# Kernel tuning notes

Measured on AMD Instinct MI355X. Metric: run time of the kernel, lower is better.

## Reference

```python
import jax, jax.numpy as jnp
import numpy as np

B, N, C, H, L, WSZ = 4, 16384, 1024, 16, 256, 512
Dh = C // H
Nb = N // B
NW = Nb // WSZ
EPS = 1e-6
SCALE = Dh ** -0.5


def _ln(h, g=None, b=None):
    m = h.mean(-1, keepdims=True)
    v = h.var(-1, keepdims=True)
    h = (h - m) * jax.lax.rsqrt(v + EPS)
    if g is not None:
        h = h * g + b
    return h


def setup_inputs() -> dict:
    key = jax.random.key(0)
    ks = jax.random.split(key, 16)
    s = 0.02
    return {
        'x': jax.random.normal(ks[0], (N, C), jnp.float32),
        'context': jax.random.normal(ks[1], (B, L, C), jnp.float32),
        'mod': jax.random.normal(ks[2], (B, C), jnp.float32),
        'W_mod': jax.random.normal(ks[3], (C, 6 * C), jnp.float32) * s,
        'b_mod': jnp.zeros((6 * C,), jnp.float32),
        'gamma2': jnp.ones((C,), jnp.float32),
        'beta2': jnp.zeros((C,), jnp.float32),
        'W_qkv': jax.random.normal(ks[4], (C, 3 * C), jnp.float32) * s,
        'b_qkv': jnp.zeros((3 * C,), jnp.float32),
        'W_so': jax.random.normal(ks[5], (C, C), jnp.float32) * s,
        'b_so': jnp.zeros((C,), jnp.float32),
        'W_q': jax.random.normal(ks[6], (C, C), jnp.float32) * s,
        'b_q': jnp.zeros((C,), jnp.float32),
        'W_kv': jax.random.normal(ks[7], (C, 2 * C), jnp.float32) * s,
        'b_kv': jnp.zeros((2 * C,), jnp.float32),
        'W_co': jax.random.normal(ks[8], (C, C), jnp.float32) * s,
        'b_co': jnp.zeros((C,), jnp.float32),
        'W_m1': jax.random.normal(ks[9], (C, 4 * C), jnp.float32) * s,
        'b_m1': jnp.zeros((4 * C,), jnp.float32),
        'W_m2': jax.random.normal(ks[10], (4 * C, C), jnp.float32) * s,
        'b_m2': jnp.zeros((C,), jnp.float32),
    }


def reference(x, context, mod, W_mod, b_mod, gamma2, beta2, W_qkv, b_qkv,
              W_so, b_so, W_q, b_q, W_kv, b_kv, W_co, b_co,
              W_m1, b_m1, W_m2, b_m2):
    xb = x.reshape(B, Nb, C)

    # AdaLN modulation: SiLU -> Linear -> 6 chunks, broadcast per batch item
    m6 = jax.nn.silu(mod) @ W_mod + b_mod                   # [B, 6C]
    sh_msa, sc_msa, g_msa, sh_mlp, sc_mlp, g_mlp = jnp.split(m6, 6, axis=-1)

    # --- windowed sparse self-attention ---
    h = _ln(xb) * (1.0 + sc_msa[:, None]) + sh_msa[:, None]
    qkv = (h @ W_qkv + b_qkv).reshape(B, NW, WSZ, 3, H, Dh)
    q, k, v = qkv[:, :, :, 0], qkv[:, :, :, 1], qkv[:, :, :, 2]
    a = jax.nn.softmax(jnp.einsum('bwqhd,bwkhd->bwhqk', q, k) * SCALE, axis=-1)
    o = jnp.einsum('bwhqk,bwkhd->bwqhd', a, v).reshape(B, Nb, C)
    xb = xb + g_msa[:, None] * (o @ W_so + b_so)

    # --- full cross-attention to per-batch context ---
    h = _ln(xb, gamma2, beta2)
    q = (h @ W_q + b_q).reshape(B, Nb, H, Dh)
    kv = (context @ W_kv + b_kv).reshape(B, L, 2, H, Dh)
    k, v = kv[:, :, 0], kv[:, :, 1]
    a = jax.nn.softmax(jnp.einsum('bqhd,bkhd->bhqk', q, k) * SCALE, axis=-1)
    o = jnp.einsum('bhqk,bkhd->bqhd', a, v).reshape(B, Nb, C)
    xb = xb + (o @ W_co + b_co)

    # --- modulated sparse FFN ---
    h = _ln(xb) * (1.0 + sc_mlp[:, None]) + sh_mlp[:, None]
    h = jax.nn.gelu(h @ W_m1 + b_m1, approximate=True)
    xb = xb + g_mlp[:, None] * (h @ W_m2 + b_m2)

    return xb.reshape(N, C)
```

## Files before the change

### kernel.cpp

```cpp
#include <hip/hip_runtime.h>

typedef unsigned short u16;
typedef __attribute__((ext_vector_type(8))) short short8;
typedef __attribute__((ext_vector_type(4))) float f32x4;

#define SCALE_ 0.125f

struct __align__(8) U16x4 { u16 x, y, z, w; };

__device__ __forceinline__ u16 f2b(float f) {
  union { float f; unsigned u; } c; c.f = f;
  unsigned u = c.u;
  u += 0x7fffu + ((u >> 16) & 1u);
  return (u16)(u >> 16);
}

__device__ __forceinline__ void gload16(const void* g, void* l) {
  __builtin_amdgcn_global_load_lds((const __attribute__((address_space(1))) void*)g,
                                   (__attribute__((address_space(3))) void*)l,
                                   16, 0, 0);
}

__device__ __forceinline__ float gelu_t(float x) {
  float z = 1.5957691216057308f * (x + 0.044715f * x * x * x);
  return x / (1.0f + __expf(-z));
}

__global__ __launch_bounds__(256) void wcast(const float* __restrict__ W,
                                             u16* __restrict__ Wt, int K, int N) {
  __shared__ float t[32][33];
  const int nb = N >> 5;
  const int k0 = (blockIdx.x / nb) << 5;
  const int n0 = (blockIdx.x % nb) << 5;
  const int tx = threadIdx.x & 31;
  const int ty = threadIdx.x >> 5;
#pragma unroll
  for (int r = 0; r < 32; r += 8) t[ty + r][tx] = W[(size_t)(k0 + ty + r) * N + n0 + tx];
  __syncthreads();
#pragma unroll
  for (int r = 0; r < 32; r += 8) Wt[(size_t)(n0 + ty + r) * K + k0 + tx] = f2b(t[tx][ty + r]);
}

__global__ __launch_bounds__(256) void cast_bf(const float* __restrict__ in,
                                               u16* __restrict__ out) {
  const int i = blockIdx.x * 256 + threadIdx.x;
  const float4 v = ((const float4*)in)[i];
  U16x4 o; o.x = f2b(v.x); o.y = f2b(v.y); o.z = f2b(v.z); o.w = f2b(v.w);
  ((U16x4*)out)[i] = o;
}

__global__ __launch_bounds__(256) void mod_gemm(const float* __restrict__ mod,
                                                const float* __restrict__ Wm,
                                                const float* __restrict__ bm,
                                                float* __restrict__ m6) {
  __shared__ float s[4096];
  for (int i = threadIdx.x; i < 4096; i += 256) {
    float x = mod[i];
    s[i] = x / (1.0f + __expf(-x));
  }
  __syncthreads();
  const int j = blockIdx.x * 256 + threadIdx.x;
  float a0 = bm[j], a1 = a0, a2 = a0, a3 = a0;
#pragma unroll 8
  for (int c = 0; c < 1024; c++) {
    float w = Wm[(size_t)c * 6144 + j];
    a0 += s[c] * w;
    a1 += s[1024 + c] * w;
    a2 += s[2048 + c] * w;
    a3 += s[3072 + c] * w;
  }
  m6[j] = a0; m6[6144 + j] = a1; m6[12288 + j] = a2; m6[18432 + j] = a3;
}

__global__ __launch_bounds__(256) void ln_k(const float* __restrict__ x,
                                            u16* __restrict__ out,
                                            const float* __restrict__ g,
                                            const float* __restrict__ bb,
                                            int batch_stride, int add_one) {
  const int row = blockIdx.x;
  const int tid = threadIdx.x;
  const float4 v = ((const float4*)(x + (size_t)row * 1024))[tid];
  float s = v.x + v.y + v.z + v.w;
  float q = v.x * v.x + v.y * v.y + v.z * v.z + v.w * v.w;
#pragma unroll
  for (int m = 1; m < 64; m <<= 1) {
    s += __shfl_xor(s, m, 64);
    q += __shfl_xor(q, m, 64);
  }
  __shared__ float ps[4], pq[4];
  if ((tid & 63) == 0) { ps[tid >> 6] = s; pq[tid >> 6] = q; }
  __syncthreads();
  s = ps[0] + ps[1] + ps[2] + ps[3];
  q = pq[0] + pq[1] + pq[2] + pq[3];
  const float mean = s * (1.0f / 1024.0f);
  const float var = q * (1.0f / 1024.0f) - mean * mean;
  const float rstd = rsqrtf(var + 1e-6f);
  const int batch = row >> 12;
  const float4 gv = ((const float4*)(g + (size_t)batch * batch_stride))[tid];
  const float4 bv = ((const float4*)(bb + (size_t)batch * batch_stride))[tid];
  const float ao = add_one ? 1.0f : 0.0f;
  U16x4 o;
  o.x = f2b((v.x - mean) * rstd * (gv.x + ao) + bv.x);
  o.y = f2b((v.y - mean) * rstd * (gv.y + ao) + bv.y);
  o.z = f2b((v.z - mean) * rstd * (gv.z + ao) + bv.z);
  o.w = f2b((v.w - mean) * rstd * (gv.w + ao) + bv.w);
  ((U16x4*)(out + (size_t)row * 1024))[tid] = o;
}

template <int EPI>
__global__ __launch_bounds__(256) void gemm_bt(const u16* __restrict__ A,
                                               const u16* __restrict__ Bt,
                                               const float* __restrict__ bias,
                                               void* outp, const float* res,
                                               const float* gate, int M, int N,
                                               int K, int gate_stride) {
  __shared__ __align__(16) u16 As[4096];
  __shared__ __align__(16) u16 Bs[4096];
  const int nb = N >> 7;
  const int bm = (blockIdx.x / nb) << 7;
  const int bn = (blockIdx.x % nb) << 7;
  const int tid = threadIdx.x;
  const int lane = tid & 63;
  const int wv = tid >> 6;
  const int wr = (wv >> 1) << 6;
  const int wc = (wv & 1) << 6;
  const int lrow = lane & 15;
  const int lk = lane >> 4;
  const int srow = tid >> 2;
  const int scol = (tid & 3) << 3;
  const u16* gA = A + (size_t)(bm + srow) * K + scol;
  const u16* gB = Bt + (size_t)(bn + srow) * K + scol;
  const size_t rskip = (size_t)64 * K;
  u16* lA = As + wv * 512;
  u16* lB = Bs + wv * 512;
  f32x4 acc[4][4] = {};
  for (int k0 = 0; k0 < K; k0 += 32) {
    gload16(gA + k0, lA);
    gload16(gA + k0 + rskip, lA + 2048);
    gload16(gB + k0, lB);
    gload16(gB + k0 + rskip, lB + 2048);
    __syncthreads();
    short8 a[4], b[4];
#pragma unroll
    for (int m = 0; m < 4; m++)
      a[m] = *(const short8*)(As + (wr + m * 16 + lrow) * 32 + lk * 8);
#pragma unroll
    for (int n = 0; n < 4; n++)
      b[n] = *(const short8*)(Bs + (wc + n * 16 + lrow) * 32 + lk * 8);
#pragma unroll
    for (int m = 0; m < 4; m++)
#pragma unroll
      for (int n = 0; n < 4; n++)
        acc[m][n] = __builtin_amdgcn_mfma_f32_16x16x32_bf16(a[m], b[n], acc[m][n], 0, 0, 0);
    __syncthreads();
  }
#pragma unroll
  for (int m = 0; m < 4; m++) {
    const int row0 = bm + wr + m * 16 + lk * 4;
#pragma unroll
    for (int n = 0; n < 4; n++) {
      const int col = bn + wc + n * 16 + lrow;
      const float bval = bias[col];
#pragma unroll
      for (int j = 0; j < 4; j++) {
        float v = acc[m][n][j] + bval;
        size_t idx = (size_t)(row0 + j) * N + col;
        ((u16*)outp)[idx] = f2b(v);
      }
    }
  }
}

template <int EPI>
__global__ __launch_bounds__(512, 4) void gemm2b(const u16* __restrict__ A,
                                                 const u16* __restrict__ Bt,
                                                 const float* __restrict__ bias,
                                                 void* outp, const float* res,
                                                 const float* gate, int M, int N,
                                                 int K, int gate_stride) {
  extern __shared__ char smem[];
  const int nb = N >> 8;
  const int nwg = (M >> 7) * nb;
  const int cpx = nwg >> 3;
  const int wg = (blockIdx.x & 7) * cpx + (blockIdx.x >> 3);
  const int bm = (wg / nb) << 7;
  const int bn = (wg % nb) << 8;
  const int tid = threadIdx.x;
  const int lane = tid & 63;
  const int w = tid >> 6;
  const int wm = w >> 2;
  const int wn = w & 3;
  const int lrow = lane & 15;
  const int lk = lane >> 4;
  const int u = (lane & 7) ^ (lane >> 3);
  const int r_off = w * 16 + ((lane >> 3) << 1) + (u >> 2);
  const int c_off = (u & 3) << 3;
  const u16* gA = A + (size_t)(bm + r_off) * K + c_off;
  const u16* gB = Bt + (size_t)(bn + r_off) * K + c_off;
  const size_t l_skip = (size_t)128 * K;
  char* sA = smem;
  char* sB = smem + 24576;
  const int dsb = ((lrow >> 1) << 7) + (((((lrow & 1) << 2) + lk) ^ (lrow >> 1)) << 4);
  const int aQ = wm * 4096;
  const int bQ = wn * 4096;

  f32x4 acc[4][4] = {};
  short8 af[4], bq[4];

#define SG(d, tt)                                                               \
  { gload16(gA + (size_t)(tt) * 32, sA + (d) * 8192 + w * 1024);                \
    gload16(gB + (size_t)(tt) * 32, sB + (d) * 16384 + w * 1024);               \
    gload16(gB + l_skip + (size_t)(tt) * 32, sB + (d) * 16384 + (w + 8) * 1024); }
#define RD_A(d)                                                                 \
  _Pragma("unroll") for (int m = 0; m < 4; m++)                                 \
    af[m] = *(const short8*)(sA + (d) * 8192 + aQ + m * 1024 + dsb);
#define RD_B(d)                                                                 \
  _Pragma("unroll") for (int n = 0; n < 4; n++)                                 \
    bq[n] = *(const short8*)(sB + (d) * 16384 + bQ + n * 1024 + dsb);
#define MM                                                                      \
  _Pragma("unroll") for (int m = 0; m < 4; m++)                                 \
    _Pragma("unroll") for (int n = 0; n < 4; n++)                               \
      acc[m][n] = __builtin_amdgcn_mfma_f32_16x16x32_bf16(af[m], bq[n], acc[m][n], 0, 0, 0);
#define SBAR0 __builtin_amdgcn_sched_barrier(0)
#define LGKM0 asm volatile("s_waitcnt lgkmcnt(0)" ::: "memory")
#define VM6   asm volatile("s_waitcnt vmcnt(6)" ::: "memory")

  const int nt = K >> 5;
  SG(0, 0);
  SG(1, (1 < nt) ? 1 : 0);
  int d = 0;
  for (int t = 0; t < nt; ++t) {
    const int d2 = (d + 2 >= 3) ? d - 1 : d + 2;
    const int tn = (t + 2 < nt) ? t + 2 : nt - 1;
    SG(d2, tn);
    SBAR0;
    VM6;
    __builtin_amdgcn_s_barrier();
    RD_A(d); RD_B(d);
    LGKM0; SBAR0;
    __builtin_amdgcn_s_setprio(1);
    MM;
    __builtin_amdgcn_s_setprio(0);
    SBAR0;
    __builtin_amdgcn_s_barrier();
    d = (d + 1 >= 3) ? 0 : d + 1;
  }
  asm volatile("s_waitcnt vmcnt(0)" ::: "memory");
#undef SG
#undef RD_A
#undef RD_B
#undef MM
#undef SBAR0
#undef LGKM0
#undef VM6

  const float* grow = nullptr;
  if (EPI == 2 && gate) grow = gate + (size_t)(bm >> 12) * gate_stride;
#pragma unroll
  for (int m = 0; m < 4; m++) {
    const int row0 = bm + wm * 64 + m * 16 + lk * 4;
#pragma unroll
    for (int n = 0; n < 4; n++) {
      const int col = bn + wn * 64 + n * 16 + lrow;
      const float bval = bias[col];
      float gval = 1.0f;
      if (EPI == 2 && grow) gval = grow[col];
#pragma unroll
      for (int j = 0; j < 4; j++) {
        float v = acc[m][n][j] + bval;
        size_t idx = (size_t)(row0 + j) * N + col;
        if (EPI == 0) {
          ((u16*)outp)[idx] = f2b(v);
        } else if (EPI == 1) {
          ((u16*)outp)[idx] = f2b(gelu_t(v));
        } else {
          ((float*)outp)[idx] = res[idx] + gval * v;
        }
      }
    }
  }
}

template <int MODE>
__global__ __launch_bounds__(512) void attn_k(const u16* __restrict__ QKV,
                                              const u16* __restrict__ Q2,
                                              const u16* __restrict__ KV2,
                                              u16* __restrict__ O) {
  __shared__ __align__(16) u16 Ks[4096];
  __shared__ __align__(16) u16 Vt[4096];
  __shared__ __align__(16) u16 Ps[16384];
  const int bid = blockIdx.x;
  const int tid = threadIdx.x;
  const int lane = tid & 63;
  const int wv = tid >> 6;
  const int lrow = lane & 15;
  const int lk = lane >> 4;
  const u16 *qp, *kp, *vp;
  int q_row0, q_stride, kv_row0, kv_stride, nkt, ocol;
  if (MODE == 0) {
    const int qt = bid & 1, h = (bid >> 1) & 15, w = (bid >> 5) & 7, b = bid >> 8;
    const int win = (b * 8 + w) * 512;
    q_row0 = win + qt * 256; q_stride = 3072;
    qp = QKV + h * 64;
    kp = QKV + 1024 + h * 64;
    vp = QKV + 2048 + h * 64;
    kv_row0 = win; kv_stride = 3072; nkt = 8;
    ocol = h * 64;
  } else {
    const int qt = bid & 15, h = (bid >> 4) & 15, b = bid >> 8;
    q_row0 = b * 4096 + qt * 256; q_stride = 1024;
    qp = Q2 + h * 64;
    kp = KV2 + h * 64;
    vp = KV2 + 1024 + h * 64;
    kv_row0 = b * 256; kv_stride = 2048; nkt = 4;
    ocol = h * 64;
  }
  const int qr = q_row0 + wv * 32;
  short8 qf[2][2];
#pragma unroll
  for (int m = 0; m < 2; m++)
#pragma unroll
    for (int kk = 0; kk < 2; kk++)
      qf[m][kk] = *(const short8*)(qp + (size_t)(qr + m * 16 + lrow) * q_stride + kk * 32 + lk * 8);
  f32x4 oa[2][4] = {};
  float lst[2][4];
#pragma unroll
  for (int m = 0; m < 2; m++)
#pragma unroll
    for (int j = 0; j < 4; j++) lst[m][j] = 0.0f;

  u16* Pw = Ps + wv * 2048;
  for (int kt = 0; kt < nkt; kt++) {
    const int kvr = kv_row0 + kt * 64;
    {
      const int r = tid >> 3, c = tid & 7;
      gload16(kp + (size_t)(kvr + r) * kv_stride + (((c) ^ (r & 7)) << 3),
              Ks + wv * 512);
    }
    {
      const int krow = tid >> 3, d0 = (tid & 7) << 3;
      short8 vvv = *(const short8*)(vp + (size_t)(kvr + krow) * kv_stride + d0);
#pragma unroll
      for (int i = 0; i < 8; i++) {
        const int ii = (i + (tid & 7)) & 7;
        const int dd = d0 + ii;
        Vt[dd * 64 + (((krow >> 3) ^ (dd & 7)) << 3) + (krow & 7)] = (u16)vvv[ii];
      }
    }
    __syncthreads();
    f32x4 s[2][4] = {};
    __builtin_amdgcn_s_setprio(1);
#pragma unroll
    for (int n = 0; n < 4; n++)
#pragma unroll
      for (int kk = 0; kk < 2; kk++) {
        short8 kb = *(const short8*)(Ks + (n * 16 + lrow) * 64 + (((kk * 4 + lk) ^ (lrow & 7)) << 3));
        s[0][n] = __builtin_amdgcn_mfma_f32_16x16x32_bf16(qf[0][kk], kb, s[0][n], 0, 0, 0);
        s[1][n] = __builtin_amdgcn_mfma_f32_16x16x32_bf16(qf[1][kk], kb, s[1][n], 0, 0, 0);
      }
    __builtin_amdgcn_s_setprio(0);
#pragma unroll
    for (int m = 0; m < 2; m++)
#pragma unroll
      for (int j = 0; j < 4; j++) {
        const float p0 = __expf(s[m][0][j] * SCALE_);
        const float p1 = __expf(s[m][1][j] * SCALE_);
        const float p2 = __expf(s[m][2][j] * SCALE_);
        const float p3 = __expf(s[m][3][j] * SCALE_);
        lst[m][j] += p0 + p1 + p2 + p3;
        const int prow = m * 16 + lk * 4 + j;
        const int base = prow * 64;
        const int r7 = prow & 7;
        const int kl = lrow >> 3, k7 = lrow & 7;
        Pw[base + (((0 + kl) ^ r7) << 3) + k7] = f2b(p0);
        Pw[base + (((2 + kl) ^ r7) << 3) + k7] = f2b(p1);
        Pw[base + (((4 + kl) ^ r7) << 3) + k7] = f2b(p2);
        Pw[base + (((6 + kl) ^ r7) << 3) + k7] = f2b(p3);
      }
#pragma unroll
    for (int kk = 0; kk < 2; kk++) {
      const int sw = ((kk * 4 + lk) ^ (lrow & 7)) << 3;
      short8 pa0 = *(const short8*)(Pw + lrow * 64 + sw);
      short8 pa1 = *(const short8*)(Pw + (16 + lrow) * 64 + sw);
      __builtin_amdgcn_s_setprio(1);
#pragma unroll
      for (int dn = 0; dn < 4; dn++) {
        short8 vb = *(const short8*)(Vt + (dn * 16 + lrow) * 64 + sw);
        oa[0][dn] = __builtin_amdgcn_mfma_f32_16x16x32_bf16(pa0, vb, oa[0][dn], 0, 0, 0);
        oa[1][dn] = __builtin_amdgcn_mfma_f32_16x16x32_bf16(pa1, vb, oa[1][dn], 0, 0, 0);
      }
      __builtin_amdgcn_s_setprio(0);
    }
    __syncthreads();
  }
#pragma unroll
  for (int m = 0; m < 2; m++)
#pragma unroll
    for (int j = 0; j < 4; j++) {
      float rs = lst[m][j];
      rs += __shfl_xor(rs, 1, 64);
      rs += __shfl_xor(rs, 2, 64);
      rs += __shfl_xor(rs, 4, 64);
      rs += __shfl_xor(rs, 8, 64);
      const float inv = 1.0f / rs;
      const int orow = qr + m * 16 + lk * 4 + j;
#pragma unroll
      for (int dn = 0; dn < 4; dn++)
        O[(size_t)orow * 1024 + ocol + dn * 16 + lrow] = f2b(oa[m][dn][j] * inv);
    }
}

extern "C" void kernel_launch(void* const* d_in, const int* in_sizes, int n_in,
                              void* d_out, int out_size, void* d_ws, size_t ws_size,
                              hipStream_t stream) {
  (void)in_sizes; (void)n_in; (void)out_size; (void)ws_size;
  const float* x      = (const float*)d_in[0];
  const float* ctx    = (const float*)d_in[1];
  const float* mod    = (const float*)d_in[2];
  const float* W_mod  = (const float*)d_in[3];
  const float* b_mod  = (const float*)d_in[4];
  const float* gamma2 = (const float*)d_in[5];
  const float* beta2  = (const float*)d_in[6];
  const float* W_qkv  = (const float*)d_in[7];
  const float* b_qkv  = (const float*)d_in[8];
  const float* W_so   = (const float*)d_in[9];
  const float* b_so   = (const float*)d_in[10];
  const float* W_q    = (const float*)d_in[11];
  const float* b_q    = (const float*)d_in[12];
  const float* W_kv   = (const float*)d_in[13];
  const float* b_kv   = (const float*)d_in[14];
  const float* W_co   = (const float*)d_in[15];
  const float* b_co   = (const float*)d_in[16];
  const float* W_m1   = (const float*)d_in[17];
  const float* b_m1   = (const float*)d_in[18];
  const float* W_m2   = (const float*)d_in[19];
  const float* b_m2   = (const float*)d_in[20];

  char* ws = (char*)d_ws;
  u16*   wt_qkv = (u16*)(ws + 0);
  u16*   wt_so  = (u16*)(ws + 6291456);
  u16*   wt_q   = (u16*)(ws + 8388608);
  u16*   wt_kv  = (u16*)(ws + 10485760);
  u16*   wt_co  = (u16*)(ws + 14680064);
  u16*   wt_m1  = (u16*)(ws + 16777216);
  u16*   wt_m2  = (u16*)(ws + 25165824);
  float* m6     = (float*)(ws + 33554432);
  u16*   ctxb   = (u16*)(ws + 33652736);
  u16*   kvb    = (u16*)(ws + 35749888);
  u16*   bufH   = (u16*)(ws + 39944192);
  u16*   bufO   = (u16*)(ws + 73498624);
  u16*   bufA   = (u16*)(ws + 107053056);
  float* xb1    = (float*)(ws + 107053056 + 50331648);
  float* outp   = (float*)d_out;

  hipFuncSetAttribute(reinterpret_cast<const void*>(&gemm2b<0>),
                      hipFuncAttributeMaxDynamicSharedMemorySize, 73728);
  hipFuncSetAttribute(reinterpret_cast<const void*>(&gemm2b<1>),
                      hipFuncAttributeMaxDynamicSharedMemorySize, 73728);
  hipFuncSetAttribute(reinterpret_cast<const void*>(&gemm2b<2>),
                      hipFuncAttributeMaxDynamicSharedMemorySize, 73728);

  wcast<<<3072, 256, 0, stream>>>(W_qkv, wt_qkv, 1024, 3072);
  wcast<<<1024, 256, 0, stream>>>(W_so,  wt_so,  1024, 1024);
  wcast<<<1024, 256, 0, stream>>>(W_q,   wt_q,   1024, 1024);
  wcast<<<2048, 256, 0, stream>>>(W_kv,  wt_kv,  1024, 2048);
  wcast<<<1024, 256, 0, stream>>>(W_co,  wt_co,  1024, 1024);
  wcast<<<4096, 256, 0, stream>>>(W_m1,  wt_m1,  1024, 4096);
  wcast<<<4096, 256, 0, stream>>>(W_m2,  wt_m2,  4096, 1024);
  cast_bf<<<1024, 256, 0, stream>>>(ctx, ctxb);

  mod_gemm<<<24, 256, 0, stream>>>(mod, W_mod, b_mod, m6);

  ln_k<<<16384, 256, 0, stream>>>(x, bufH, m6 + 1024, m6 + 0, 6144, 1);
  gemm2b<0><<<1536, 512, 73728, stream>>>(bufH, wt_qkv, b_qkv, bufA, nullptr, nullptr, 16384, 3072, 1024, 0);
  attn_k<0><<<1024, 512, 0, stream>>>(bufA, nullptr, nullptr, bufO);
  gemm2b<2><<<512, 512, 73728, stream>>>(bufO, wt_so, b_so, xb1, x, m6 + 2048, 16384, 1024, 1024, 6144);

  ln_k<<<16384, 256, 0, stream>>>(xb1, bufH, gamma2, beta2, 0, 0);
  gemm2b<0><<<512, 512, 73728, stream>>>(bufH, wt_q, b_q, bufA, nullptr, nullptr, 16384, 1024, 1024, 0);
  gemm_bt<0><<<128, 256, 0, stream>>>(ctxb, wt_kv, b_kv, kvb, nullptr, nullptr, 1024, 2048, 1024, 0);
  attn_k<1><<<1024, 512, 0, stream>>>(nullptr, bufA, kvb, bufO);
  gemm2b<2><<<512, 512, 73728, stream>>>(bufO, wt_co, b_co, outp, xb1, nullptr, 16384, 1024, 1024, 0);

  ln_k<<<16384, 256, 0, stream>>>(outp, bufH, m6 + 4096, m6 + 3072, 6144, 1);
  gemm2b<1><<<2048, 512, 73728, stream>>>(bufH, wt_m1, b_m1, bufA, nullptr, nullptr, 16384, 4096, 1024, 0);
  gemm2b<2><<<512, 512, 73728, stream>>>(bufA, wt_m2, b_m2, outp, outp, m6 + 5120, 16384, 1024, 4096, 6144);
}
```

Baseline: 1.003 ms.

## Enlarge GEMM tile to 256x256 with split A-half MFMA pipelining

```diff
diff --git a/kernel.cpp b/kernel.cpp
--- a/kernel.cpp
+++ b/kernel.cpp
@@ -172,18 +172,18 @@
 }
 
 template <int EPI>
-__global__ __launch_bounds__(512, 4) void gemm2b(const u16* __restrict__ A,
-                                                 const u16* __restrict__ Bt,
-                                                 const float* __restrict__ bias,
-                                                 void* outp, const float* res,
-                                                 const float* gate, int M, int N,
-                                                 int K, int gate_stride) {
+__global__ __launch_bounds__(512, 2) void gemm8(const u16* __restrict__ A,
+                                                const u16* __restrict__ Bt,
+                                                const float* __restrict__ bias,
+                                                void* outp, const float* res,
+                                                const float* gate, int M, int N,
+                                                int K, int gate_stride) {
   extern __shared__ char smem[];
   const int nb = N >> 8;
-  const int nwg = (M >> 7) * nb;
+  const int nwg = (M >> 8) * nb;
   const int cpx = nwg >> 3;
   const int wg = (blockIdx.x & 7) * cpx + (blockIdx.x >> 3);
-  const int bm = (wg / nb) << 7;
+  const int bm = (wg / nb) << 8;
   const int bn = (wg % nb) << 8;
   const int tid = threadIdx.x;
   const int lane = tid & 63;
@@ -198,67 +198,75 @@
   const u16* gA = A + (size_t)(bm + r_off) * K + c_off;
   const u16* gB = Bt + (size_t)(bn + r_off) * K + c_off;
   const size_t l_skip = (size_t)128 * K;
-  char* sA = smem;
-  char* sB = smem + 24576;
   const int dsb = ((lrow >> 1) << 7) + (((((lrow & 1) << 2) + lk) ^ (lrow >> 1)) << 4);
-  const int aQ = wm * 4096;
-  const int bQ = wn * 4096;
-
-  f32x4 acc[4][4] = {};
+  const int aQ = wm * 8192;
+  const int bQ = 16384 + wn * 4096;
+
+  f32x4 acc[8][4] = {};
   short8 af[4], bq[4];
 
-#define SG(d, tt)                                                               \
-  { gload16(gA + (size_t)(tt) * 32, sA + (d) * 8192 + w * 1024);                \
-    gload16(gB + (size_t)(tt) * 32, sB + (d) * 16384 + w * 1024);               \
-    gload16(gB + l_skip + (size_t)(tt) * 32, sB + (d) * 16384 + (w + 8) * 1024); }
-#define RD_A(d)                                                                 \
+#define SG_A(s, tt)                                                             \
+  { gload16(gA + (size_t)(tt) * 32, smem + (s) * 32768 + w * 1024);             \
+    gload16(gA + l_skip + (size_t)(tt) * 32, smem + (s) * 32768 + 8192 + w * 1024); }
+#define SG_B(s, tt)                                                             \
+  { gload16(gB + (size_t)(tt) * 32, smem + (s) * 32768 + 16384 + w * 1024);     \
+    gload16(gB + l_skip + (size_t)(tt) * 32, smem + (s) * 32768 + 24576 + w * 1024); }
+#define RD_A(s, mh)                                                             \
   _Pragma("unroll") for (int m = 0; m < 4; m++)                                 \
-    af[m] = *(const short8*)(sA + (d) * 8192 + aQ + m * 1024 + dsb);
-#define RD_B(d)                                                                 \
+    af[m] = *(const short8*)(smem + (s) * 32768 + aQ + (mh) * 4096 + m * 1024 + dsb);
+#define RD_B(s)                                                                 \
   _Pragma("unroll") for (int n = 0; n < 4; n++)                                 \
-    bq[n] = *(const short8*)(sB + (d) * 16384 + bQ + n * 1024 + dsb);
-#define MM                                                                      \
+    bq[n] = *(const short8*)(smem + (s) * 32768 + bQ + n * 1024 + dsb);
+#define MM(mh)                                                                  \
   _Pragma("unroll") for (int m = 0; m < 4; m++)                                 \
     _Pragma("unroll") for (int n = 0; n < 4; n++)                               \
-      acc[m][n] = __builtin_amdgcn_mfma_f32_16x16x32_bf16(af[m], bq[n], acc[m][n], 0, 0, 0);
+      acc[(mh) * 4 + m][n] =                                                    \
+          __builtin_amdgcn_mfma_f32_16x16x32_bf16(af[m], bq[n], acc[(mh) * 4 + m][n], 0, 0, 0);
 #define SBAR0 __builtin_amdgcn_sched_barrier(0)
 #define LGKM0 asm volatile("s_waitcnt lgkmcnt(0)" ::: "memory")
-#define VM6   asm volatile("s_waitcnt vmcnt(6)" ::: "memory")
-
+#define VM4   asm volatile("s_waitcnt vmcnt(4)" ::: "memory")
+
+  SG_A(0, 0); SG_B(0, 0); SG_A(1, 1); SG_B(1, 1);
   const int nt = K >> 5;
-  SG(0, 0);
-  SG(1, (1 < nt) ? 1 : 0);
-  int d = 0;
+  int s0 = 0;
   for (int t = 0; t < nt; ++t) {
-    const int d2 = (d + 2 >= 3) ? d - 1 : d + 2;
+    int s2 = s0 + 2; if (s2 >= 3) s2 -= 3;
     const int tn = (t + 2 < nt) ? t + 2 : nt - 1;
-    SG(d2, tn);
     SBAR0;
-    VM6;
+    VM4;
     __builtin_amdgcn_s_barrier();
-    RD_A(d); RD_B(d);
+    SBAR0;
+    SG_A(s2, tn);
+    RD_A(s0, 0); RD_B(s0);
     LGKM0; SBAR0;
     __builtin_amdgcn_s_setprio(1);
-    MM;
+    MM(0);
     __builtin_amdgcn_s_setprio(0);
     SBAR0;
-    __builtin_amdgcn_s_barrier();
-    d = (d + 1 >= 3) ? 0 : d + 1;
+    SG_B(s2, tn);
+    RD_A(s0, 1);
+    LGKM0; SBAR0;
+    __builtin_amdgcn_s_setprio(1);
+    MM(1);
+    __builtin_amdgcn_s_setprio(0);
+    SBAR0;
+    s0 = (s0 + 1 >= 3) ? 0 : s0 + 1;
   }
   asm volatile("s_waitcnt vmcnt(0)" ::: "memory");
-#undef SG
+#undef SG_A
+#undef SG_B
 #undef RD_A
 #undef RD_B
 #undef MM
 #undef SBAR0
 #undef LGKM0
-#undef VM6
+#undef VM4
 
   const float* grow = nullptr;
   if (EPI == 2 && gate) grow = gate + (size_t)(bm >> 12) * gate_stride;
 #pragma unroll
-  for (int m = 0; m < 4; m++) {
-    const int row0 = bm + wm * 64 + m * 16 + lk * 4;
+  for (int m = 0; m < 8; m++) {
+    const int row0 = bm + wm * 128 + m * 16 + lk * 4;
 #pragma unroll
     for (int n = 0; n < 4; n++) {
       const int col = bn + wn * 64 + n * 16 + lrow;
@@ -453,12 +461,12 @@
   float* xb1    = (float*)(ws + 107053056 + 50331648);
   float* outp   = (float*)d_out;
 
-  hipFuncSetAttribute(reinterpret_cast<const void*>(&gemm2b<0>),
-                      hipFuncAttributeMaxDynamicSharedMemorySize, 73728);
-  hipFuncSetAttribute(reinterpret_cast<const void*>(&gemm2b<1>),
-                      hipFuncAttributeMaxDynamicSharedMemorySize, 73728);
-  hipFuncSetAttribute(reinterpret_cast<const void*>(&gemm2b<2>),
-                      hipFuncAttributeMaxDynamicSharedMemorySize, 73728);
+  hipFuncSetAttribute(reinterpret_cast<const void*>(&gemm8<0>),
+                      hipFuncAttributeMaxDynamicSharedMemorySize, 98304);
+  hipFuncSetAttribute(reinterpret_cast<const void*>(&gemm8<1>),
+                      hipFuncAttributeMaxDynamicSharedMemorySize, 98304);
+  hipFuncSetAttribute(reinterpret_cast<const void*>(&gemm8<2>),
+                      hipFuncAttributeMaxDynamicSharedMemorySize, 98304);
 
   wcast<<<3072, 256, 0, stream>>>(W_qkv, wt_qkv, 1024, 3072);
   wcast<<<1024, 256, 0, stream>>>(W_so,  wt_so,  1024, 1024);
@@ -472,17 +480,17 @@
   mod_gemm<<<24, 256, 0, stream>>>(mod, W_mod, b_mod, m6);
 
   ln_k<<<16384, 256, 0, stream>>>(x, bufH, m6 + 1024, m6 + 0, 6144, 1);
-  gemm2b<0><<<1536, 512, 73728, stream>>>(bufH, wt_qkv, b_qkv, bufA, nullptr, nullptr, 16384, 3072, 1024, 0);
+  gemm8<0><<<768, 512, 98304, stream>>>(bufH, wt_qkv, b_qkv, bufA, nullptr, nullptr, 16384, 3072, 1024, 0);
   attn_k<0><<<1024, 512, 0, stream>>>(bufA, nullptr, nullptr, bufO);
-  gemm2b<2><<<512, 512, 73728, stream>>>(bufO, wt_so, b_so, xb1, x, m6 + 2048, 16384, 1024, 1024, 6144);
+  gemm8<2><<<256, 512, 98304, stream>>>(bufO, wt_so, b_so, xb1, x, m6 + 2048, 16384, 1024, 1024, 6144);
 
   ln_k<<<16384, 256, 0, stream>>>(xb1, bufH, gamma2, beta2, 0, 0);
-  gemm2b<0><<<512, 512, 73728, stream>>>(bufH, wt_q, b_q, bufA, nullptr, nullptr, 16384, 1024, 1024, 0);
+  gemm8<0><<<256, 512, 98304, stream>>>(bufH, wt_q, b_q, bufA, nullptr, nullptr, 16384, 1024, 1024, 0);
   gemm_bt<0><<<128, 256, 0, stream>>>(ctxb, wt_kv, b_kv, kvb, nullptr, nullptr, 1024, 2048, 1024, 0);
   attn_k<1><<<1024, 512, 0, stream>>>(nullptr, bufA, kvb, bufO);
-  gemm2b<2><<<512, 512, 73728, stream>>>(bufO, wt_co, b_co, outp, xb1, nullptr, 16384, 1024, 1024, 0);
+  gemm8<2><<<256, 512, 98304, stream>>>(bufO, wt_co, b_co, outp, xb1, nullptr, 16384, 1024, 1024, 0);
 
   ln_k<<<16384, 256, 0, stream>>>(outp, bufH, m6 + 4096, m6 + 3072, 6144, 1);
-  gemm2b<1><<<2048, 512, 73728, stream>>>(bufH, wt_m1, b_m1, bufA, nullptr, nullptr, 16384, 4096, 1024, 0);
-  gemm2b<2><<<512, 512, 73728, stream>>>(bufA, wt_m2, b_m2, outp, outp, m6 + 5120, 16384, 1024, 4096, 6144);
-}
+  gemm8<1><<<1024, 512, 98304, stream>>>(bufH, wt_m1, b_m1, bufA, nullptr, nullptr, 16384, 4096, 1024, 0);
+  gemm8<2><<<256, 512, 98304, stream>>>(bufA, wt_m2, b_m2, outp, outp, m6 + 5120, 16384, 1024, 4096, 6144);
+}
```

Result: no change. 1.018 ms (+1.4%).
